# Kernel tuning notes

Hardware: AMD Instinct MI355X
Metric: run time of the kernel (lower is better)

The kernel has to match this reference:

```python
import jax, jax.numpy as jnp
import numpy as np

N_NODE = 4096
N_FEA_IN = 128
N_FEA_OUT = 128


def setup_inputs() -> dict:
    key = jax.random.key(0)
    k_x, k_a, k_w, k_att = jax.random.split(key, 4)
    stdv_w = 1.0 / np.sqrt(N_FEA_OUT)       # torch reset: 1/sqrt(W.size(1))
    stdv_a = 1.0 / np.sqrt(2 * N_FEA_OUT)   # a is [1, 2*n_fea_out]
    X = jax.random.normal(k_x, (N_NODE, N_FEA_IN), dtype=jnp.float32)
    A = jax.random.uniform(k_a, (N_NODE, N_NODE), dtype=jnp.float32)  # dense weighted adjacency
    W = jax.random.uniform(k_w, (N_FEA_IN, N_FEA_OUT), minval=-stdv_w, maxval=stdv_w, dtype=jnp.float32)
    a = jax.random.uniform(k_att, (1, 2 * N_FEA_OUT), minval=-stdv_a, maxval=stdv_a, dtype=jnp.float32)
    return {"X": X, "A": A, "W": W, "a": a}


def reference(X, A, W, a):
    # XW: [N, F_out]
    XW = jnp.matmul(X, W)
    f = W.shape[1]
    # Z[i,j] = concat(XW[j], XW[i]); Z @ a.T decomposes into two rank-1 broadcasts:
    s_col = jnp.matmul(XW, a[0, :f])   # depends on column index j
    s_row = jnp.matmul(XW, a[0, f:])   # depends on row index i
    Z1 = jax.nn.leaky_relu(s_row[:, None] + s_col[None, :], negative_slope=0.01)  # [N, N]
    den = jnp.exp(Z1)                  # [N, N]
    num = jnp.matmul(A, den)           # numerator[i,j] = sum_k A[i,k] * den[k,j]
    # vectorized replacement of the Python double loop: att = den/num where num != 0
    att = jnp.where(num != 0, den / jnp.where(num != 0, num, 1.0), 0.0)
    H = jnp.matmul(A, jnp.matmul(att, XW))
    return H
```

## Files before the change

### kernel.cpp

```cpp
#include <hip/hip_runtime.h>
#include <hip/hip_bf16.h>
#include <stdint.h>

#define NN 4096
#define NF 128
#define XROWS 4

using f32x4  = __attribute__((ext_vector_type(4))) float;
using bf16x8 = __attribute__((ext_vector_type(8))) __bf16;
using u16x8  = __attribute__((ext_vector_type(8))) uint16_t;

__device__ __forceinline__ uint16_t f2b(float f) {
    union { float f; uint32_t u; } v; v.f = f;
    uint32_t r = v.u + 0x7FFFu + ((v.u >> 16) & 1u);
    return (uint16_t)(r >> 16);
}

__device__ __forceinline__ float b2f(uint16_t u) {
    union { uint32_t u; float f; } v; v.u = ((uint32_t)u) << 16;
    return v.f;
}

__global__ __launch_bounds__(128) void xw_kernel(
    const float* __restrict__ X, const float* __restrict__ W,
    const float* __restrict__ a,
    uint16_t* __restrict__ XWT,
    float* __restrict__ s_col, float* __restrict__ s_row) {
    __shared__ float xs[XROWS][NF];
    __shared__ float red[XROWS][2][2];
    const int i0 = blockIdx.x * XROWS, f = threadIdx.x;
    #pragma unroll
    for (int r = 0; r < XROWS; ++r) xs[r][f] = X[(size_t)(i0 + r) * NF + f];
    __syncthreads();
    float acc[XROWS] = {0.f, 0.f, 0.f, 0.f};
    #pragma unroll 4
    for (int k = 0; k < NF; ++k) {
        const float w = W[k * NF + f];
        #pragma unroll
        for (int r = 0; r < XROWS; ++r) acc[r] += xs[r][k] * w;
    }
    ushort4 xo;
    xo.x = f2b(acc[0]); xo.y = f2b(acc[1]); xo.z = f2b(acc[2]); xo.w = f2b(acc[3]);
    *(ushort4*)(XWT + (size_t)f * NN + i0) = xo;
    const float a1 = a[f], a2 = a[NF + f];
    #pragma unroll
    for (int r = 0; r < XROWS; ++r) {
        float sc = acc[r] * a1;
        float sr = acc[r] * a2;
        #pragma unroll
        for (int off = 32; off; off >>= 1) {
            sc += __shfl_down(sc, off);
            sr += __shfl_down(sr, off);
        }
        if ((f & 63) == 0) { red[r][f >> 6][0] = sc; red[r][f >> 6][1] = sr; }
    }
    __syncthreads();
    if (f < XROWS) {
        s_col[i0 + f] = red[f][0][0] + red[f][1][0];
        s_row[i0 + f] = red[f][0][1] + red[f][1][1];
    }
}

__global__ __launch_bounds__(256) void prep_kernel(
    const float* __restrict__ s_row, const float* __restrict__ s_col,
    int* __restrict__ ks, float* __restrict__ w1s, float* __restrict__ w2s,
    float4* __restrict__ rec) {
    __shared__ __align__(16) float sr[NN];
    const int t = threadIdx.x;
    #pragma unroll
    for (int c = 0; c < 16; ++c) sr[t + c * 256] = s_row[t + c * 256];
    __syncthreads();
    const bool isC = blockIdx.x >= 128;
    const int tgt = (blockIdx.x & 127) * 32 + (t >> 3);
    const int sub = t & 7;
    const float4* sr4 = (const float4*)sr;
    int cnt = 0;
    if (!isC) {
        const float s = sr[tgt];
        #pragma unroll 4
        for (int q = 0; q < 128; ++q) {
            const int k4 = q * 8 + sub;
            float4 v = sr4[k4];
            const int kb = k4 * 4;
            cnt += (v.x < s) | ((v.x == s) & (kb + 0 < tgt));
            cnt += (v.y < s) | ((v.y == s) & (kb + 1 < tgt));
            cnt += (v.z < s) | ((v.z == s) & (kb + 2 < tgt));
            cnt += (v.w < s) | ((v.w == s) & (kb + 3 < tgt));
        }
    } else {
        const float th = -s_col[tgt];
        #pragma unroll 4
        for (int q = 0; q < 128; ++q) {
            float4 v = sr4[q * 8 + sub];
            cnt += (v.x <= th) + (v.y <= th) + (v.z <= th) + (v.w <= th);
        }
    }
    cnt += __shfl_down(cnt, 4);
    cnt += __shfl_down(cnt, 2);
    cnt += __shfl_down(cnt, 1);
    if (sub == 0) {
        if (!isC) {
            const float s = sr[tgt];
            ks[cnt]  = tgt;
            w1s[cnt] = __expf(s);
            w2s[cnt] = __expf(0.01f * s);
        } else {
            const float sc = s_col[tgt];
            rec[tgt] = (float4){__int_as_float(cnt), __expf(sc), __expf(0.01f * sc), sc};
        }
    }
}

#define PB(b) ((b) + (((b) >> 4) << 1))

__global__ __launch_bounds__(512, 8) void row_kernel(
    const float* __restrict__ A,
    const float* __restrict__ s_row,
    const int* __restrict__ ks, const float* __restrict__ w1s, const float* __restrict__ w2s,
    const float4* __restrict__ rec,
    uint16_t* __restrict__ Ab, uint16_t* __restrict__ att) {
    __shared__ __align__(16) float rowA[NN];
    __shared__ __align__(16) uint16_t S1[4640];
    __shared__ __align__(16) uint16_t S2[4640];
    __shared__ float wtot[2][8];
    const int i = blockIdx.x, t = threadIdx.x;

    {
        const float4* Ar = (const float4*)(A + (size_t)i * NN);
        ushort4* Abr = (ushort4*)(Ab + (size_t)i * NN);
        #pragma unroll
        for (int c = 0; c < 2; ++c) {
            float4 v = Ar[t + c * 512];
            ((float4*)rowA)[t + c * 512] = v;
            ushort4 o; o.x = f2b(v.x); o.y = f2b(v.y); o.z = f2b(v.z); o.w = f2b(v.w);
            Abr[t + c * 512] = o;
        }
    }
    __syncthreads();

    float l1[8], l2[8];
    {
        const int4*   k4 = (const int4*)ks;
        const float4* a4 = (const float4*)w1s;
        const float4* b4 = (const float4*)w2s;
        float run1 = 0.f, run2 = 0.f;
        #pragma unroll
        for (int g = 0; g < 2; ++g) {
            int4   kk = k4[2 * t + g];
            float4 wa = a4[2 * t + g];
            float4 wb = b4[2 * t + g];
            float g0 = rowA[kk.x], g1 = rowA[kk.y], g2 = rowA[kk.z], g3 = rowA[kk.w];
            run1 += g0 * wa.x; l1[4 * g + 0] = run1;  run2 += g0 * wb.x; l2[4 * g + 0] = run2;
            run1 += g1 * wa.y; l1[4 * g + 1] = run1;  run2 += g1 * wb.y; l2[4 * g + 1] = run2;
            run1 += g2 * wa.z; l1[4 * g + 2] = run1;  run2 += g2 * wb.z; l2[4 * g + 2] = run2;
            run1 += g3 * wa.w; l1[4 * g + 3] = run1;  run2 += g3 * wb.w; l2[4 * g + 3] = run2;
        }
    }
    float s1 = l1[7], s2 = l2[7];
    const int lane = t & 63, wid = t >> 6;
    #pragma unroll
    for (int off = 1; off < 64; off <<= 1) {
        float u1 = __shfl_up(s1, off);
        float u2 = __shfl_up(s2, off);
        if (lane >= off) { s1 += u1; s2 += u2; }
    }
    if (lane == 63) { wtot[0][wid] = s1; wtot[1][wid] = s2; }
    __syncthreads();

    float off1 = 0.f, off2 = 0.f, tot1 = 0.f, tot2 = 0.f;
    #pragma unroll
    for (int w = 0; w < 8; ++w) {
        const float va = wtot[0][w], vb = wtot[1][w];
        tot1 += va; tot2 += vb;
        if (w < wid) { off1 += va; off2 += vb; }
    }
    const float ex1 = off1 + s1 - l1[7];
    const float ex2 = off2 + s2 - l2[7];
    {
        uint32_t* q1 = (uint32_t*)S1;
        uint32_t* q2 = (uint32_t*)S2;
        const int qb = t * 4 + (t >> 1);
        #pragma unroll
        for (int m = 0; m < 4; ++m) {
            const float pl1 = m ? l1[2 * m - 1] : 0.f;
            const float pl2 = m ? l2[2 * m - 1] : 0.f;
            const float sa = tot1 - ex1 - pl1;
            const float sb = tot1 - ex1 - l1[2 * m];
            const float pa = ex2 + pl2;
            const float pb = ex2 + l2[2 * m];
            q1[qb + m] = (uint32_t)f2b(sa) | ((uint32_t)f2b(sb) << 16);
            q2[qb + m] = (uint32_t)f2b(pa) | ((uint32_t)f2b(pb) << 16);
        }
    }
    if (t == 511) {
        S1[PB(4096)] = 0;
        S2[PB(4096)] = f2b(tot2);
    }
    __syncthreads();

    const float sri = s_row[i];
    uint32_t* attR = (uint32_t*)(att + (size_t)i * NN);
    #pragma unroll
    for (int e = 0; e < 4; ++e) {
        const int j0 = e * 1024 + 2 * t;
        const float4 ra = rec[j0];
        const float4 rb = rec[j0 + 1];
        const int Ca = __float_as_int(ra.x);
        const int Cb = __float_as_int(rb.x);
        const float numa = ra.y * b2f(S1[PB(Ca)]) + ra.z * b2f(S2[PB(Ca)]);
        const float numb = rb.y * b2f(S1[PB(Cb)]) + rb.z * b2f(S2[PB(Cb)]);
        float za = sri + ra.w; za = za > 0.f ? za : 0.01f * za;
        float zb = sri + rb.w; zb = zb > 0.f ? zb : 0.01f * zb;
        const float dena = __expf(za);
        const float denb = __expf(zb);
        const float va = (numa != 0.f) ? dena * __builtin_amdgcn_rcpf(numa) : 0.f;
        const float vb = (numb != 0.f) ? denb * __builtin_amdgcn_rcpf(numb) : 0.f;
        attR[e * 512 + t] = (uint32_t)f2b(va) | ((uint32_t)f2b(vb) << 16);
    }
}

__device__ __forceinline__ void gemm16_core(
    const uint16_t* __restrict__ Aop, const uint16_t* __restrict__ Bop,
    int i0, float* __restrict__ red, float2* __restrict__ v) {
    const int t = threadIdx.x;
    const int lane = t & 63, wv = t >> 6;
    const int l16 = lane & 15, quad = lane >> 4;
    const int kBeg = wv * 256;

    f32x4 acc[8];
    #pragma unroll
    for (int ni = 0; ni < 8; ++ni) acc[ni] = (f32x4){0.f, 0.f, 0.f, 0.f};

    const uint16_t* Ap = Aop + (size_t)(i0 + l16) * NN + quad * 8;
    const uint16_t* Bp = Bop + (size_t)l16 * NN + quad * 8;

    #pragma unroll
    for (int kk = 0; kk < 256; kk += 32) {
        const int k0 = kBeg + kk;
        const bf16x8 af = *(const bf16x8*)(Ap + k0);
        #pragma unroll
        for (int ni = 0; ni < 8; ++ni) {
            const bf16x8 bf = *(const bf16x8*)(Bp + (size_t)(ni * 16) * NN + k0);
            acc[ni] = __builtin_amdgcn_mfma_f32_16x16x32_bf16(af, bf, acc[ni], 0, 0, 0);
        }
    }

    float* img = red + (wv & 3) * 2048;
    const int base = l16 * 16 + quad * 4;
    #pragma unroll
    for (int ph = 0; ph < 4; ++ph) {
        if ((wv >> 2) == ph) {
            if (ph == 0) {
                #pragma unroll
                for (int ni = 0; ni < 8; ++ni)
                    *(f32x4*)(img + ni * 256 + base) = acc[ni];
            } else {
                #pragma unroll
                for (int ni = 0; ni < 8; ++ni) {
                    f32x4 x = *(const f32x4*)(img + ni * 256 + base);
                    *(f32x4*)(img + ni * 256 + base) = x + acc[ni];
                }
            }
        }
        __syncthreads();
    }
    float2 s = {0.f, 0.f};
    #pragma unroll
    for (int im = 0; im < 4; ++im) {
        const float2 x = *(const float2*)(red + im * 2048 + 2 * t);
        s.x += x.x; s.y += x.y;
    }
    *v = s;
}

__global__ __launch_bounds__(1024, 4) void gemm_fused_m1(
    const uint16_t* __restrict__ Aop, const uint16_t* __restrict__ Bop,
    uint16_t* __restrict__ M1T) {
    __shared__ __align__(16) float red[4 * 2048];
    const int i0 = blockIdx.x * 16;
    float2 v;
    gemm16_core(Aop, Bop, i0, red, &v);
    const int p = 2 * threadIdx.x;
    const int f = p >> 4, il = p & 15;
    ushort2 o; o.x = f2b(v.x); o.y = f2b(v.y);
    *(ushort2*)(M1T + (size_t)f * NN + i0 + il) = o;
}

__global__ __launch_bounds__(1024, 4) void gemm_fused_h(
    const uint16_t* __restrict__ Aop, const uint16_t* __restrict__ Bop,
    float* __restrict__ H) {
    __shared__ __align__(16) float red[4 * 2048];
    __shared__ __align__(16) float lds2[16][132];
    const int i0 = blockIdx.x * 16;
    float2 v;
    gemm16_core(Aop, Bop, i0, red, &v);
    const int p = 2 * threadIdx.x;
    const int f = p >> 4, il = p & 15;
    lds2[il][f] = v.x;
    lds2[il + 1][f] = v.y;
    __syncthreads();
    const int t = threadIdx.x;
    if (t < 512) {
        const int r = t >> 5, fq = t & 31;
        const float4 x = *(const float4*)(&lds2[r][fq * 4]);
        *(float4*)(H + (size_t)(i0 + r) * NF + fq * 4) = x;
    }
}

extern "C" void kernel_launch(void* const* d_in, const int* in_sizes, int n_in,
                              void* d_out, int out_size, void* d_ws, size_t ws_size,
                              hipStream_t stream) {
    (void)in_sizes; (void)n_in; (void)out_size; (void)ws_size;
    const float* X = (const float*)d_in[0];
    const float* A = (const float*)d_in[1];
    const float* W = (const float*)d_in[2];
    const float* a = (const float*)d_in[3];
    float* H = (float*)d_out;

    char* ws = (char*)d_ws;
    uint16_t* Ab  = (uint16_t*)(ws);
    uint16_t* att = (uint16_t*)(ws + ((size_t)32 << 20));
    uint16_t* XWT = (uint16_t*)(ws + ((size_t)96 << 20));
    uint16_t* M1T = (uint16_t*)(ws + ((size_t)97 << 20));
    char* sm = ws + ((size_t)64 << 20);
    float*  s_col = (float*) (sm);
    float*  s_row = (float*) (sm + (16 << 10));
    int*    ks    = (int*)   (sm + (32 << 10));
    float*  w1s   = (float*) (sm + (48 << 10));
    float*  w2s   = (float*) (sm + (64 << 10));
    float4* rec   = (float4*)(sm + (80 << 10));

    xw_kernel<<<NN / XROWS, NF, 0, stream>>>(X, W, a, XWT, s_col, s_row);
    prep_kernel<<<256, 256, 0, stream>>>(s_row, s_col, ks, w1s, w2s, rec);
    row_kernel<<<NN, 512, 0, stream>>>(A, s_row, ks, w1s, w2s, rec, Ab, att);
    gemm_fused_m1<<<NN / 16, 1024, 0, stream>>>(att, XWT, M1T);
    gemm_fused_h<<<NN / 16, 1024, 0, stream>>>(Ab, M1T, H);
}
```

Baseline: 217.4 us.

## Drop bf16 copy of A; convert fp32 A on the fly in final GEMM

row_kernel no longer writes a bf16 copy of A (32 MB), and the final GEMM instead reads fp32 A directly, converting to bf16 in registers before the MFMA. This removes a 32 MB write and trades a 32 MB bf16 read for a 64 MB fp32 read, so the net traffic drops by 32 MB. The row kernel also hoists its loads of ks, w1s, w2s and rec to the top so they overlap with the A row load. Conversion ALU work is added to the GEMM's inner loop.

```diff
diff --git a/kernel.cpp b/kernel.cpp
--- a/kernel.cpp
+++ b/kernel.cpp
@@ -118,43 +118,48 @@
     const float* __restrict__ s_row,
     const int* __restrict__ ks, const float* __restrict__ w1s, const float* __restrict__ w2s,
     const float4* __restrict__ rec,
-    uint16_t* __restrict__ Ab, uint16_t* __restrict__ att) {
+    uint16_t* __restrict__ att) {
     __shared__ __align__(16) float rowA[NN];
     __shared__ __align__(16) uint16_t S1[4640];
     __shared__ __align__(16) uint16_t S2[4640];
     __shared__ float wtot[2][8];
     const int i = blockIdx.x, t = threadIdx.x;
 
+    const float sri = s_row[i];
+    const int4   kk0 = ((const int4*)ks)[2 * t];
+    const int4   kk1 = ((const int4*)ks)[2 * t + 1];
+    const float4 wa0 = ((const float4*)w1s)[2 * t];
+    const float4 wa1 = ((const float4*)w1s)[2 * t + 1];
+    const float4 wb0 = ((const float4*)w2s)[2 * t];
+    const float4 wb1 = ((const float4*)w2s)[2 * t + 1];
+    float4 ra[4], rb[4];
+    #pragma unroll
+    for (int e = 0; e < 4; ++e) {
+        ra[e] = rec[e * 1024 + 2 * t];
+        rb[e] = rec[e * 1024 + 2 * t + 1];
+    }
+
     {
         const float4* Ar = (const float4*)(A + (size_t)i * NN);
-        ushort4* Abr = (ushort4*)(Ab + (size_t)i * NN);
-        #pragma unroll
-        for (int c = 0; c < 2; ++c) {
-            float4 v = Ar[t + c * 512];
-            ((float4*)rowA)[t + c * 512] = v;
-            ushort4 o; o.x = f2b(v.x); o.y = f2b(v.y); o.z = f2b(v.z); o.w = f2b(v.w);
-            Abr[t + c * 512] = o;
-        }
+        #pragma unroll
+        for (int c = 0; c < 2; ++c)
+            ((float4*)rowA)[t + c * 512] = Ar[t + c * 512];
     }
     __syncthreads();
 
     float l1[8], l2[8];
     {
-        const int4*   k4 = (const int4*)ks;
-        const float4* a4 = (const float4*)w1s;
-        const float4* b4 = (const float4*)w2s;
         float run1 = 0.f, run2 = 0.f;
-        #pragma unroll
-        for (int g = 0; g < 2; ++g) {
-            int4   kk = k4[2 * t + g];
-            float4 wa = a4[2 * t + g];
-            float4 wb = b4[2 * t + g];
-            float g0 = rowA[kk.x], g1 = rowA[kk.y], g2 = rowA[kk.z], g3 = rowA[kk.w];
-            run1 += g0 * wa.x; l1[4 * g + 0] = run1;  run2 += g0 * wb.x; l2[4 * g + 0] = run2;
-            run1 += g1 * wa.y; l1[4 * g + 1] = run1;  run2 += g1 * wb.y; l2[4 * g + 1] = run2;
-            run1 += g2 * wa.z; l1[4 * g + 2] = run1;  run2 += g2 * wb.z; l2[4 * g + 2] = run2;
-            run1 += g3 * wa.w; l1[4 * g + 3] = run1;  run2 += g3 * wb.w; l2[4 * g + 3] = run2;
-        }
+        float g0 = rowA[kk0.x], g1 = rowA[kk0.y], g2 = rowA[kk0.z], g3 = rowA[kk0.w];
+        run1 += g0 * wa0.x; l1[0] = run1;  run2 += g0 * wb0.x; l2[0] = run2;
+        run1 += g1 * wa0.y; l1[1] = run1;  run2 += g1 * wb0.y; l2[1] = run2;
+        run1 += g2 * wa0.z; l1[2] = run1;  run2 += g2 * wb0.z; l2[2] = run2;
+        run1 += g3 * wa0.w; l1[3] = run1;  run2 += g3 * wb0.w; l2[3] = run2;
+        g0 = rowA[kk1.x]; g1 = rowA[kk1.y]; g2 = rowA[kk1.z]; g3 = rowA[kk1.w];
+        run1 += g0 * wa1.x; l1[4] = run1;  run2 += g0 * wb1.x; l2[4] = run2;
+        run1 += g1 * wa1.y; l1[5] = run1;  run2 += g1 * wb1.y; l2[5] = run2;
+        run1 += g2 * wa1.z; l1[6] = run1;  run2 += g2 * wb1.z; l2[6] = run2;
+        run1 += g3 * wa1.w; l1[7] = run1;  run2 += g3 * wb1.w; l2[7] = run2;
     }
     float s1 = l1[7], s2 = l2[7];
     const int lane = t & 63, wid = t >> 6;
@@ -198,19 +203,15 @@
     }
     __syncthreads();
 
-    const float sri = s_row[i];
     uint32_t* attR = (uint32_t*)(att + (size_t)i * NN);
     #pragma unroll
     for (int e = 0; e < 4; ++e) {
-        const int j0 = e * 1024 + 2 * t;
-        const float4 ra = rec[j0];
-        const float4 rb = rec[j0 + 1];
-        const int Ca = __float_as_int(ra.x);
-        const int Cb = __float_as_int(rb.x);
-        const float numa = ra.y * b2f(S1[PB(Ca)]) + ra.z * b2f(S2[PB(Ca)]);
-        const float numb = rb.y * b2f(S1[PB(Cb)]) + rb.z * b2f(S2[PB(Cb)]);
-        float za = sri + ra.w; za = za > 0.f ? za : 0.01f * za;
-        float zb = sri + rb.w; zb = zb > 0.f ? zb : 0.01f * zb;
+        const int Ca = __float_as_int(ra[e].x);
+        const int Cb = __float_as_int(rb[e].x);
+        const float numa = ra[e].y * b2f(S1[PB(Ca)]) + ra[e].z * b2f(S2[PB(Ca)]);
+        const float numb = rb[e].y * b2f(S1[PB(Cb)]) + rb[e].z * b2f(S2[PB(Cb)]);
+        float za = sri + ra[e].w; za = za > 0.f ? za : 0.01f * za;
+        float zb = sri + rb[e].w; zb = zb > 0.f ? zb : 0.01f * zb;
         const float dena = __expf(za);
         const float denb = __expf(zb);
         const float va = (numa != 0.f) ? dena * __builtin_amdgcn_rcpf(numa) : 0.f;
@@ -219,32 +220,11 @@
     }
 }
 
-__device__ __forceinline__ void gemm16_core(
-    const uint16_t* __restrict__ Aop, const uint16_t* __restrict__ Bop,
-    int i0, float* __restrict__ red, float2* __restrict__ v) {
+__device__ __forceinline__ void gemm16_reduce(
+    float* __restrict__ red, const f32x4 acc[8], float2* __restrict__ v) {
     const int t = threadIdx.x;
     const int lane = t & 63, wv = t >> 6;
     const int l16 = lane & 15, quad = lane >> 4;
-    const int kBeg = wv * 256;
-
-    f32x4 acc[8];
-    #pragma unroll
-    for (int ni = 0; ni < 8; ++ni) acc[ni] = (f32x4){0.f, 0.f, 0.f, 0.f};
-
-    const uint16_t* Ap = Aop + (size_t)(i0 + l16) * NN + quad * 8;
-    const uint16_t* Bp = Bop + (size_t)l16 * NN + quad * 8;
-
-    #pragma unroll
-    for (int kk = 0; kk < 256; kk += 32) {
-        const int k0 = kBeg + kk;
-        const bf16x8 af = *(const bf16x8*)(Ap + k0);
-        #pragma unroll
-        for (int ni = 0; ni < 8; ++ni) {
-            const bf16x8 bf = *(const bf16x8*)(Bp + (size_t)(ni * 16) * NN + k0);
-            acc[ni] = __builtin_amdgcn_mfma_f32_16x16x32_bf16(af, bf, acc[ni], 0, 0, 0);
-        }
-    }
-
     float* img = red + (wv & 3) * 2048;
     const int base = l16 * 16 + quad * 4;
     #pragma unroll
@@ -278,28 +258,76 @@
     uint16_t* __restrict__ M1T) {
     __shared__ __align__(16) float red[4 * 2048];
     const int i0 = blockIdx.x * 16;
+    const int t = threadIdx.x;
+    const int lane = t & 63, wv = t >> 6;
+    const int l16 = lane & 15, quad = lane >> 4;
+    const int kBeg = wv * 256;
+
+    f32x4 acc[8];
+    #pragma unroll
+    for (int ni = 0; ni < 8; ++ni) acc[ni] = (f32x4){0.f, 0.f, 0.f, 0.f};
+
+    const uint16_t* Ap = Aop + (size_t)(i0 + l16) * NN + quad * 8;
+    const uint16_t* Bp = Bop + (size_t)l16 * NN + quad * 8;
+
+    #pragma unroll
+    for (int kk = 0; kk < 256; kk += 32) {
+        const int k0 = kBeg + kk;
+        const bf16x8 af = *(const bf16x8*)(Ap + k0);
+        #pragma unroll
+        for (int ni = 0; ni < 8; ++ni) {
+            const bf16x8 bf = *(const bf16x8*)(Bp + (size_t)(ni * 16) * NN + k0);
+            acc[ni] = __builtin_amdgcn_mfma_f32_16x16x32_bf16(af, bf, acc[ni], 0, 0, 0);
+        }
+    }
     float2 v;
-    gemm16_core(Aop, Bop, i0, red, &v);
-    const int p = 2 * threadIdx.x;
+    gemm16_reduce(red, acc, &v);
+    const int p = 2 * t;
     const int f = p >> 4, il = p & 15;
     ushort2 o; o.x = f2b(v.x); o.y = f2b(v.y);
     *(ushort2*)(M1T + (size_t)f * NN + i0 + il) = o;
 }
 
 __global__ __launch_bounds__(1024, 4) void gemm_fused_h(
-    const uint16_t* __restrict__ Aop, const uint16_t* __restrict__ Bop,
+    const float* __restrict__ Aop, const uint16_t* __restrict__ Bop,
     float* __restrict__ H) {
     __shared__ __align__(16) float red[4 * 2048];
     __shared__ __align__(16) float lds2[16][132];
     const int i0 = blockIdx.x * 16;
+    const int t = threadIdx.x;
+    const int lane = t & 63, wv = t >> 6;
+    const int l16 = lane & 15, quad = lane >> 4;
+    const int kBeg = wv * 256;
+
+    f32x4 acc[8];
+    #pragma unroll
+    for (int ni = 0; ni < 8; ++ni) acc[ni] = (f32x4){0.f, 0.f, 0.f, 0.f};
+
+    const float*    Ap = Aop + (size_t)(i0 + l16) * NN + quad * 8;
+    const uint16_t* Bp = Bop + (size_t)l16 * NN + quad * 8;
+
+    #pragma unroll
+    for (int kk = 0; kk < 256; kk += 32) {
+        const int k0 = kBeg + kk;
+        const float4 va = *(const float4*)(Ap + k0);
+        const float4 vb = *(const float4*)(Ap + k0 + 4);
+        union { uint16_t u[8]; bf16x8 v; } afu;
+        afu.u[0] = f2b(va.x); afu.u[1] = f2b(va.y); afu.u[2] = f2b(va.z); afu.u[3] = f2b(va.w);
+        afu.u[4] = f2b(vb.x); afu.u[5] = f2b(vb.y); afu.u[6] = f2b(vb.z); afu.u[7] = f2b(vb.w);
+        const bf16x8 af = afu.v;
+        #pragma unroll
+        for (int ni = 0; ni < 8; ++ni) {
+            const bf16x8 bf = *(const bf16x8*)(Bp + (size_t)(ni * 16) * NN + k0);
+            acc[ni] = __builtin_amdgcn_mfma_f32_16x16x32_bf16(af, bf, acc[ni], 0, 0, 0);
+        }
+    }
     float2 v;
-    gemm16_core(Aop, Bop, i0, red, &v);
-    const int p = 2 * threadIdx.x;
+    gemm16_reduce(red, acc, &v);
+    const int p = 2 * t;
     const int f = p >> 4, il = p & 15;
     lds2[il][f] = v.x;
     lds2[il + 1][f] = v.y;
     __syncthreads();
-    const int t = threadIdx.x;
     if (t < 512) {
         const int r = t >> 5, fq = t & 31;
         const float4 x = *(const float4*)(&lds2[r][fq * 4]);
@@ -318,7 +346,6 @@
     float* H = (float*)d_out;
 
     char* ws = (char*)d_ws;
-    uint16_t* Ab  = (uint16_t*)(ws);
     uint16_t* att = (uint16_t*)(ws + ((size_t)32 << 20));
     uint16_t* XWT = (uint16_t*)(ws + ((size_t)96 << 20));
     uint16_t* M1T = (uint16_t*)(ws + ((size_t)97 << 20));
@@ -332,7 +359,7 @@
 
     xw_kernel<<<NN / XROWS, NF, 0, stream>>>(X, W, a, XWT, s_col, s_row);
     prep_kernel<<<256, 256, 0, stream>>>(s_row, s_col, ks, w1s, w2s, rec);
-    row_kernel<<<NN, 512, 0, stream>>>(A, s_row, ks, w1s, w2s, rec, Ab, att);
+    row_kernel<<<NN, 512, 0, stream>>>(A, s_row, ks, w1s, w2s, rec, att);
     gemm_fused_m1<<<NN / 16, 1024, 0, stream>>>(att, XWT, M1T);
-    gemm_fused_h<<<NN / 16, 1024, 0, stream>>>(Ab, M1T, H);
-}
+    gemm_fused_h<<<NN / 16, 1024, 0, stream>>>(A, M1T, H);
+}
```

New measurement: 271.2 us. 24.8% more time.
